# Performance work log

Measured on AMD Instinct MI355X. Metric: run time of the kernel, lower is better.

## Reference

```python
import jax, jax.numpy as jnp
import numpy as np

B, S, D_IN, D_OUT = 8, 2048, 1024, 1024

def setup_inputs() -> dict:
    key = jax.random.key(0)
    k1, k2, k3, k4 = jax.random.split(key, 4)
    sc = 0.02
    return {
        "x": jax.random.normal(k1, (B, S, D_IN), dtype=jnp.float32),
        "Wq": jax.random.normal(k2, (D_IN, D_OUT), dtype=jnp.float32) * sc,
        "Wk": jax.random.normal(k3, (D_IN, D_OUT), dtype=jnp.float32) * sc,
        "Wv": jax.random.normal(k4, (D_IN, D_OUT), dtype=jnp.float32) * sc,
    }

def reference(x, Wq, Wk, Wv):
    b, n, _ = x.shape
    d_out = Wq.shape[1]
    q = jnp.einsum('bsd,de->bse', x, Wq)   # [b, n, d_out]
    k = jnp.einsum('bsd,de->bse', x, Wk)
    v = jnp.einsum('bsd,de->bse', x, Wv)
    scores = jnp.einsum('bie,bje->bij', q, k)  # [b, n, n]
    # causal mask: positions j > i set to -inf (triu, diagonal=1)
    causal = jnp.triu(jnp.ones((n, n), dtype=bool), k=1)
    scores = jnp.where(causal[None, :, :], -jnp.inf, scores)
    # NOTE: source applies softmax over dim=1 (query axis), scaled by sqrt(d_out)
    weights = jax.nn.softmax(scores / jnp.sqrt(jnp.float32(d_out)), axis=1)
    # dropout is identity in eval mode (p=0)
    return jnp.einsum('bij,bje->bie', weights, v)
```

## Files before the change

kernel.cpp:

```cpp
#include <hip/hip_runtime.h>
#include <hip/hip_bf16.h>


using bf16 = __hip_bfloat16;
typedef __attribute__((ext_vector_type(8))) short short8;
typedef __attribute__((ext_vector_type(4))) float f32x4;

__device__ __forceinline__ float bfbits2f(unsigned short u) {
  return __uint_as_float((unsigned)u << 16);
}

__global__ void cvt_kernel(const float* __restrict__ in, bf16* __restrict__ out) {
  size_t i = ((size_t)blockIdx.x * 256 + threadIdx.x) * 4;
  float4 v = *(const float4*)(in + i);
  alignas(8) bf16 h[4] = {__float2bfloat16(v.x), __float2bfloat16(v.y),
                          __float2bfloat16(v.z), __float2bfloat16(v.w)};
  *(unsigned long long*)(out + i) = *(const unsigned long long*)h;
}

__global__ void pre_kernel(const float* __restrict__ x,
                           const float* __restrict__ W0, const float* __restrict__ W1,
                           const float* __restrict__ W2, bf16* __restrict__ Wt,
                           float* __restrict__ lbuf, bf16* __restrict__ Xb) {
  int tid = threadIdx.x;
  int zz = blockIdx.z;
  if (zz == 3) {
    int bid = blockIdx.y * 16 + blockIdx.x;
    if (bid < 64) lbuf[bid * 256 + tid] = 0.f;
    return;
  }
  if (zz >= 4) {
    size_t cb = (size_t)(zz - 4) * 256 + blockIdx.y * 16 + blockIdx.x;
    size_t i = (cb * 256 + tid) * 4;
    float4 v = *(const float4*)(x + i);
    alignas(8) bf16 h[4] = {__float2bfloat16(v.x), __float2bfloat16(v.y),
                            __float2bfloat16(v.z), __float2bfloat16(v.w)};
    *(unsigned long long*)(Xb + i) = *(const unsigned long long*)h;
    return;
  }
  const float* W = zz == 0 ? W0 : zz == 1 ? W1 : W2;
  bf16* O = Wt + (size_t)zz * 1048576ull;
  __shared__ float t[64][65];
  int n0 = blockIdx.x * 64, k0 = blockIdx.y * 64;
#pragma unroll
  for (int i = 0; i < 4; ++i) {
    int idx = i * 1024 + tid * 4;
    int r = idx >> 6, c = idx & 63;
    float4 v = *(const float4*)(W + (size_t)(k0 + r) * 1024 + n0 + c);
    t[r][c] = v.x; t[r][c + 1] = v.y; t[r][c + 2] = v.z; t[r][c + 3] = v.w;
  }
  __syncthreads();
#pragma unroll
  for (int i = 0; i < 4; ++i) {
    int idx = i * 1024 + tid * 4;
    int r = idx >> 6, c = idx & 63;
    alignas(8) bf16 h[4] = {__float2bfloat16(t[c][r]), __float2bfloat16(t[c + 1][r]),
                            __float2bfloat16(t[c + 2][r]), __float2bfloat16(t[c + 3][r])};
    *(unsigned long long*)(O + (size_t)(n0 + r) * 1024 + k0 + c) = *(const unsigned long long*)h;
  }
}

__global__ void vhat_kernel(const bf16* __restrict__ QKV, const float* __restrict__ l,
                            bf16* __restrict__ Vt) {
  int lb = blockIdx.z;
  const unsigned short* V =
      (const unsigned short*)QKV + ((size_t)lb * 3 + 2) * 2097152ull;
  bf16* O = Vt + (size_t)lb * 2097152ull;
  const float* lc = l + lb * 2048;
  __shared__ float t[64][65];
  __shared__ float rl[64];
  int j0 = blockIdx.x * 64, e0 = blockIdx.y * 64;
  int tid = threadIdx.x;
  if (tid < 64) rl[tid] = 1.0f / lc[j0 + tid];
#pragma unroll
  for (int i = 0; i < 4; ++i) {
    int idx = i * 1024 + tid * 4;
    int r = idx >> 6, c = idx & 63;
    ushort4 u = *(const ushort4*)(V + (size_t)(j0 + r) * 1024 + e0 + c);
    t[r][c] = bfbits2f(u.x); t[r][c + 1] = bfbits2f(u.y);
    t[r][c + 2] = bfbits2f(u.z); t[r][c + 3] = bfbits2f(u.w);
  }
  __syncthreads();
#pragma unroll
  for (int i = 0; i < 4; ++i) {
    int idx = i * 1024 + tid * 4;
    int r = idx >> 6, c = idx & 63;
    alignas(8) bf16 h[4] = {
        __float2bfloat16(t[c][r] * rl[c]), __float2bfloat16(t[c + 1][r] * rl[c + 1]),
        __float2bfloat16(t[c + 2][r] * rl[c + 2]), __float2bfloat16(t[c + 3][r] * rl[c + 3])};
    *(unsigned long long*)(O + (size_t)(e0 + r) * 2048 + j0 + c) = *(const unsigned long long*)h;
  }
}

template <int EPI, bool VARK, bool TRI>
__device__ __forceinline__ void gemm_bt_body(
    const bf16* __restrict__ A, const bf16* __restrict__ B, void* __restrict__ Cv,
    int lda, int ldb, int ldc, int Kin, int zdivA, int zmodB,
    unsigned long long sA, unsigned long long sB, unsigned long long sC,
    float* __restrict__ lptr) {
  unsigned bz, bx, by;
  if constexpr (TRI) {
    const unsigned gx = gridDim.x;
    const unsigned total = gx * gridDim.z;
    unsigned id = blockIdx.x + gx * blockIdx.z;
    unsigned lid = (id & 7) * (total >> 3) + (id >> 3);
    bz = lid / gx;
    unsigned t = lid - bz * gx;
    int r = (int)((__builtin_sqrtf(8.f * (float)t + 1.f) - 1.f) * 0.5f);
    while ((r + 1) * (r + 2) / 2 <= (int)t) ++r;
    while (r * (r + 1) / 2 > (int)t) --r;
    by = (unsigned)r;
    bx = t - (unsigned)(r * (r + 1) / 2);
  } else {
    const unsigned gx = gridDim.x, gy = gridDim.y;
    const unsigned per_z = gx * gy;
    const unsigned total = per_z * gridDim.z;
    unsigned id = blockIdx.x + gx * (blockIdx.y + gy * blockIdx.z);
    unsigned lid = (id & 7) * (total >> 3) + (id >> 3);
    bz = lid / per_z;
    unsigned rem = lid - bz * per_z;
    constexpr unsigned H = 8;
    const unsigned band = rem / (gx * H);
    const unsigned w = rem - band * (gx * H);
    bx = w / H;
    const unsigned by_raw = band * H + (w - bx * H);
    by = VARK ? (gy - 1 - by_raw) : by_raw;
  }

  const int z = (int)bz;
  A += (unsigned long long)(z / zdivA) * sA;
  B += (unsigned long long)(z % zmodB) * sB;
  const int K = VARK ? (int)(by + 1) * 128 : Kin;

  alignas(16) __shared__ bf16 As[128 * 64];
  alignas(16) __shared__ bf16 Bs[128 * 64];

  const int tid = threadIdx.x, wave = tid >> 6, lane = tid & 63;
  const int m0 = by * 128, n0 = bx * 128;
  const int srow = tid >> 3;
  const int scol_g = ((tid & 7) ^ (srow & 7)) * 8;
  const int scol_l = (tid & 7) * 8;
  const int wm = (wave >> 1) * 64, wn = (wave & 1) * 64;
  const int fm = lane & 15, sw = lane & 7, kg = lane >> 4;

  f32x4 acc[4][4];
#pragma unroll
  for (int mi = 0; mi < 4; ++mi)
#pragma unroll
    for (int ni = 0; ni < 4; ++ni) acc[mi][ni] = (f32x4){0.f, 0.f, 0.f, 0.f};

  const bf16* Arow = A + (size_t)m0 * lda;
  const bf16* Brow = B + (size_t)n0 * ldb;

  for (int k0 = 0; k0 < K; k0 += 64) {
    __syncthreads();
#pragma unroll
    for (int c = 0; c < 4; ++c) {
      int row = c * 32 + srow;
      __builtin_amdgcn_global_load_lds(
          (const __attribute__((address_space(1))) void*)(Arow + (size_t)row * lda + k0 + scol_g),
          (__attribute__((address_space(3))) void*)(As + row * 64 + scol_l), 16, 0, 0);
    }
#pragma unroll
    for (int c = 0; c < 4; ++c) {
      int row = c * 32 + srow;
      __builtin_amdgcn_global_load_lds(
          (const __attribute__((address_space(1))) void*)(Brow + (size_t)row * ldb + k0 + scol_g),
          (__attribute__((address_space(3))) void*)(Bs + row * 64 + scol_l), 16, 0, 0);
    }
    __syncthreads();
#pragma unroll
    for (int ks = 0; ks < 2; ++ks) {
      const int pc = ((ks * 4 + kg) ^ sw) * 8;
      short8 af[4], bf_[4];
#pragma unroll
      for (int i = 0; i < 4; ++i) {
        af[i] = *(const short8*)(As + (wm + i * 16 + fm) * 64 + pc);
        bf_[i] = *(const short8*)(Bs + (wn + i * 16 + fm) * 64 + pc);
      }
#pragma unroll
      for (int mi = 0; mi < 4; ++mi)
#pragma unroll
        for (int ni = 0; ni < 4; ++ni)
          acc[mi][ni] = __builtin_amdgcn_mfma_f32_16x16x32_bf16(af[mi], bf_[ni], acc[mi][ni], 0, 0, 0);
    }
  }

  const int cr = kg * 4, cc = fm;
  if constexpr (EPI == 2) {
    float* C = (float*)Cv + (unsigned long long)z * sC;
#pragma unroll
    for (int mi = 0; mi < 4; ++mi)
#pragma unroll
      for (int ni = 0; ni < 4; ++ni)
#pragma unroll
        for (int r = 0; r < 4; ++r)
          C[(size_t)(m0 + wm + mi * 16 + cr + r) * ldc + (n0 + wn + ni * 16 + cc)] = acc[mi][ni][r];
  } else if constexpr (EPI == 0) {
    bf16* C = (bf16*)Cv + (unsigned long long)z * sC;
#pragma unroll
    for (int mi = 0; mi < 4; ++mi)
#pragma unroll
      for (int ni = 0; ni < 4; ++ni)
#pragma unroll
        for (int r = 0; r < 4; ++r)
          C[(size_t)(m0 + wm + mi * 16 + cr + r) * ldc + (n0 + wn + ni * 16 + cc)] =
              __float2bfloat16(acc[mi][ni][r]);
  } else {
    bf16* C = (bf16*)Cv + (unsigned long long)z * sC;
    float colpart[4] = {0.f, 0.f, 0.f, 0.f};
#pragma unroll
    for (int mi = 0; mi < 4; ++mi)
#pragma unroll
      for (int ni = 0; ni < 4; ++ni)
#pragma unroll
        for (int r = 0; r < 4; ++r) {
          int gm = m0 + wm + mi * 16 + cr + r;
          int gn = n0 + wn + ni * 16 + cc;
          float s = acc[mi][ni][r] * 0.03125f;
          float p = (gn <= gm) ? __expf(s) : 0.f;
          colpart[ni] += p;
          C[(size_t)gm * ldc + gn] = __float2bfloat16(p);
        }
    float* lcol = lptr + (size_t)z * 2048 + n0 + wn;
#pragma unroll
    for (int ni = 0; ni < 4; ++ni) {
      float s = colpart[ni];
      s += __shfl_xor(s, 16);
      s += __shfl_xor(s, 32);
      if (lane < 16) atomicAdd(&lcol[ni * 16 + lane], s);
    }
  }
}

__global__ __launch_bounds__(256, 4) void gemm_qkv(
    const bf16* __restrict__ A, const bf16* __restrict__ B, void* __restrict__ Cv,
    int lda, int ldb, int ldc, int Kin, int zdivA, int zmodB,
    unsigned long long sA, unsigned long long sB, unsigned long long sC) {
  gemm_bt_body<0, false, false>(A, B, Cv, lda, ldb, ldc, Kin, zdivA, zmodB, sA, sB, sC, nullptr);
}
__global__ __launch_bounds__(256, 4) void gemm_scores(
    const bf16* __restrict__ A, const bf16* __restrict__ B, void* __restrict__ Cv,
    int lda, int ldb, int ldc, int Kin, int zdivA, int zmodB,
    unsigned long long sA, unsigned long long sB, unsigned long long sC,
    float* __restrict__ lptr) {
  gemm_bt_body<1, false, true>(A, B, Cv, lda, ldb, ldc, Kin, zdivA, zmodB, sA, sB, sC, lptr);
}
__global__ __launch_bounds__(256, 4) void gemm_pv(
    const bf16* __restrict__ A, const bf16* __restrict__ B, void* __restrict__ Cv,
    int lda, int ldb, int ldc, int Kin, int zdivA, int zmodB,
    unsigned long long sA, unsigned long long sB, unsigned long long sC) {
  gemm_bt_body<2, true, false>(A, B, Cv, lda, ldb, ldc, Kin, zdivA, zmodB, sA, sB, sC, nullptr);
}

extern "C" void kernel_launch(void* const* d_in, const int* in_sizes, int n_in,
                              void* d_out, int out_size, void* d_ws, size_t ws_size,
                              hipStream_t stream) {
  const float* x = (const float*)d_in[0];
  const float* Wq = (const float*)d_in[1];
  const float* Wk = (const float*)d_in[2];
  const float* Wv = (const float*)d_in[3];
  float* out = (float*)d_out;

  constexpr unsigned long long X_EL = 2048ull * 1024;
  constexpr unsigned long long QKV_EL = 3ull * X_EL;
  constexpr unsigned long long P_EL = 2048ull * 2048;
  constexpr unsigned long long VT_EL = 1024ull * 2048;
  constexpr unsigned long long WT_B = 3ull * 1024 * 1024 * 2;
  constexpr unsigned long long LB_B = 8ull * 2048 * 4;
  constexpr unsigned long long PER_B = 2 * (X_EL + QKV_EL + P_EL + VT_EL);

  size_t NB = 1;
  for (size_t nb : {(size_t)8, (size_t)4, (size_t)2})
    if (WT_B + LB_B + nb * PER_B <= ws_size) { NB = nb; break; }

  char* p = (char*)d_ws;
  bf16* Wt = (bf16*)p;   p += WT_B;
  float* lbuf = (float*)p; p += LB_B;
  bf16* Xb = (bf16*)p;   p += 2 * NB * X_EL;
  bf16* QKV = (bf16*)p;  p += 2 * NB * QKV_EL;
  bf16* P = (bf16*)p;    p += 2 * NB * P_EL;
  bf16* Vt = (bf16*)p;

  pre_kernel<<<dim3(16, 16, (unsigned)(4 + NB * 8)), 256, 0, stream>>>(
      x, Wq, Wk, Wv, Wt, lbuf, Xb);

  for (size_t b0 = 0; b0 < 8; b0 += NB) {
    if (b0)
      cvt_kernel<<<dim3((unsigned)(NB * 2048)), 256, 0, stream>>>(x + b0 * X_EL, Xb);
    const size_t nbA = NB / 2, nbB = NB - nbA;
    if (nbA)
      gemm_qkv<<<dim3(8, 16, (unsigned)(nbA * 3)), 256, 0, stream>>>(
          Xb, Wt, QKV, 1024, 1024, 1024, 1024, 3, 3, X_EL, 1048576ull, X_EL);
    gemm_qkv<<<dim3(8, 16, (unsigned)(nbB * 3)), 256, 0, stream>>>(
        Xb + nbA * X_EL, Wt, QKV + nbA * QKV_EL, 1024, 1024, 1024, 1024, 3, 3,
        X_EL, 1048576ull, X_EL);
    gemm_scores<<<dim3(136, 1, (unsigned)NB), 256, 0, stream>>>(
        QKV, QKV + X_EL, P, 1024, 1024, 2048, 1024, 1, 1 << 30, QKV_EL, QKV_EL, P_EL,
        lbuf + b0 * 2048);
    vhat_kernel<<<dim3(32, 16, (unsigned)NB), 256, 0, stream>>>(QKV, lbuf + b0 * 2048, Vt);
    gemm_pv<<<dim3(8, 16, (unsigned)NB), 256, 0, stream>>>(
        P, Vt, out + b0 * X_EL, 2048, 2048, 1024, 0, 1, 1 << 30, P_EL, VT_EL, X_EL);
  }
}
```

Measured before the change: 341.7 us.

## Pair triangular row tiles in PV GEMM for balanced work per block

Rewrites the PV GEMM as a dedicated kernel with 128x64 tiles, where each block handles two row tiles (15-p and p) of the causal P matrix. Every block therefore does a constant total K length instead of the earlier varying-K 128x128 tiles, which removes tail imbalance. It also merges the two split QKV GEMM launches into one. The cost is smaller N tiles, which means less B reuse per block and more A reloads, plus a smaller accumulator tile.

```diff
diff --git a/kernel.cpp b/kernel.cpp
--- a/kernel.cpp
+++ b/kernel.cpp
@@ -92,7 +92,7 @@
   }
 }
 
-template <int EPI, bool VARK, bool TRI>
+template <int EPI, bool TRI>
 __device__ __forceinline__ void gemm_bt_body(
     const bf16* __restrict__ A, const bf16* __restrict__ B, void* __restrict__ Cv,
     int lda, int ldb, int ldc, int Kin, int zdivA, int zmodB,
@@ -123,14 +123,13 @@
     const unsigned band = rem / (gx * H);
     const unsigned w = rem - band * (gx * H);
     bx = w / H;
-    const unsigned by_raw = band * H + (w - bx * H);
-    by = VARK ? (gy - 1 - by_raw) : by_raw;
+    by = band * H + (w - bx * H);
   }
 
   const int z = (int)bz;
   A += (unsigned long long)(z / zdivA) * sA;
   B += (unsigned long long)(z % zmodB) * sB;
-  const int K = VARK ? (int)(by + 1) * 128 : Kin;
+  const int K = Kin;
 
   alignas(16) __shared__ bf16 As[128 * 64];
   alignas(16) __shared__ bf16 Bs[128 * 64];
@@ -187,16 +186,7 @@
   }
 
   const int cr = kg * 4, cc = fm;
-  if constexpr (EPI == 2) {
-    float* C = (float*)Cv + (unsigned long long)z * sC;
-#pragma unroll
-    for (int mi = 0; mi < 4; ++mi)
-#pragma unroll
-      for (int ni = 0; ni < 4; ++ni)
-#pragma unroll
-        for (int r = 0; r < 4; ++r)
-          C[(size_t)(m0 + wm + mi * 16 + cr + r) * ldc + (n0 + wn + ni * 16 + cc)] = acc[mi][ni][r];
-  } else if constexpr (EPI == 0) {
+  if constexpr (EPI == 0) {
     bf16* C = (bf16*)Cv + (unsigned long long)z * sC;
 #pragma unroll
     for (int mi = 0; mi < 4; ++mi)
@@ -237,20 +227,102 @@
     const bf16* __restrict__ A, const bf16* __restrict__ B, void* __restrict__ Cv,
     int lda, int ldb, int ldc, int Kin, int zdivA, int zmodB,
     unsigned long long sA, unsigned long long sB, unsigned long long sC) {
-  gemm_bt_body<0, false, false>(A, B, Cv, lda, ldb, ldc, Kin, zdivA, zmodB, sA, sB, sC, nullptr);
+  gemm_bt_body<0, false>(A, B, Cv, lda, ldb, ldc, Kin, zdivA, zmodB, sA, sB, sC, nullptr);
 }
 __global__ __launch_bounds__(256, 4) void gemm_scores(
     const bf16* __restrict__ A, const bf16* __restrict__ B, void* __restrict__ Cv,
     int lda, int ldb, int ldc, int Kin, int zdivA, int zmodB,
     unsigned long long sA, unsigned long long sB, unsigned long long sC,
     float* __restrict__ lptr) {
-  gemm_bt_body<1, false, true>(A, B, Cv, lda, ldb, ldc, Kin, zdivA, zmodB, sA, sB, sC, lptr);
-}
+  gemm_bt_body<1, true>(A, B, Cv, lda, ldb, ldc, Kin, zdivA, zmodB, sA, sB, sC, lptr);
+}
+
 __global__ __launch_bounds__(256, 4) void gemm_pv(
-    const bf16* __restrict__ A, const bf16* __restrict__ B, void* __restrict__ Cv,
-    int lda, int ldb, int ldc, int Kin, int zdivA, int zmodB,
+    const bf16* __restrict__ Pm, const bf16* __restrict__ Vt, float* __restrict__ out,
     unsigned long long sA, unsigned long long sB, unsigned long long sC) {
-  gemm_bt_body<2, true, false>(A, B, Cv, lda, ldb, ldc, Kin, zdivA, zmodB, sA, sB, sC, nullptr);
+  const unsigned gx = gridDim.x, gy = gridDim.y;
+  const unsigned per_z = gx * gy;
+  const unsigned total = per_z * gridDim.z;
+  unsigned id = blockIdx.x + gx * (blockIdx.y + gy * blockIdx.z);
+  unsigned lid = (id & 7) * (total >> 3) + (id >> 3);
+  const unsigned bz = lid / per_z;
+  unsigned rem = lid - bz * per_z;
+  const unsigned bx = rem >> 3;
+  const unsigned pp = rem & 7;
+  const int z = (int)bz;
+
+  const bf16* A = Pm + (unsigned long long)z * sA;
+  const bf16* B = Vt + (unsigned long long)z * sB;
+  float* C = out + (unsigned long long)z * sC;
+
+  alignas(16) __shared__ bf16 As[128 * 64];
+  alignas(16) __shared__ bf16 Bs[64 * 64];
+
+  const int tid = threadIdx.x, wave = tid >> 6, lane = tid & 63;
+  const int srow = tid >> 3;
+  const int scol_g = ((tid & 7) ^ (srow & 7)) * 8;
+  const int scol_l = (tid & 7) * 8;
+  const int wm = (wave >> 1) * 64, wn = (wave & 1) * 32;
+  const int fm = lane & 15, sw = lane & 7, kg = lane >> 4;
+  const int n0 = (int)bx * 64;
+  const bf16* Brow = B + (size_t)n0 * 2048;
+
+  auto phase = [&](int by, int K) {
+    const int m0 = by * 128;
+    const bf16* Arow = A + (size_t)m0 * 2048;
+    f32x4 acc[4][2];
+#pragma unroll
+    for (int mi = 0; mi < 4; ++mi)
+#pragma unroll
+      for (int nj = 0; nj < 2; ++nj) acc[mi][nj] = (f32x4){0.f, 0.f, 0.f, 0.f};
+
+    for (int k0 = 0; k0 < K; k0 += 64) {
+      __syncthreads();
+#pragma unroll
+      for (int c = 0; c < 4; ++c) {
+        int row = c * 32 + srow;
+        __builtin_amdgcn_global_load_lds(
+            (const __attribute__((address_space(1))) void*)(Arow + (size_t)row * 2048 + k0 + scol_g),
+            (__attribute__((address_space(3))) void*)(As + row * 64 + scol_l), 16, 0, 0);
+      }
+#pragma unroll
+      for (int c = 0; c < 2; ++c) {
+        int row = c * 32 + srow;
+        __builtin_amdgcn_global_load_lds(
+            (const __attribute__((address_space(1))) void*)(Brow + (size_t)row * 2048 + k0 + scol_g),
+            (__attribute__((address_space(3))) void*)(Bs + row * 64 + scol_l), 16, 0, 0);
+      }
+      __syncthreads();
+#pragma unroll
+      for (int ks = 0; ks < 2; ++ks) {
+        const int pc = ((ks * 4 + kg) ^ sw) * 8;
+        short8 af[4], bf_[2];
+#pragma unroll
+        for (int i = 0; i < 4; ++i)
+          af[i] = *(const short8*)(As + (wm + i * 16 + fm) * 64 + pc);
+#pragma unroll
+        for (int j = 0; j < 2; ++j)
+          bf_[j] = *(const short8*)(Bs + (wn + j * 16 + fm) * 64 + pc);
+#pragma unroll
+        for (int mi = 0; mi < 4; ++mi)
+#pragma unroll
+          for (int nj = 0; nj < 2; ++nj)
+            acc[mi][nj] = __builtin_amdgcn_mfma_f32_16x16x32_bf16(af[mi], bf_[nj], acc[mi][nj], 0, 0, 0);
+      }
+    }
+    const int cr = kg * 4, cc = fm;
+#pragma unroll
+    for (int mi = 0; mi < 4; ++mi)
+#pragma unroll
+      for (int nj = 0; nj < 2; ++nj)
+#pragma unroll
+        for (int r = 0; r < 4; ++r)
+          C[(size_t)(m0 + wm + mi * 16 + cr + r) * 1024 + (n0 + wn + nj * 16 + cc)] =
+              acc[mi][nj][r];
+  };
+
+  phase(15 - (int)pp, (16 - (int)pp) * 128);
+  phase((int)pp, ((int)pp + 1) * 128);
 }
 
 extern "C" void kernel_launch(void* const* d_in, const int* in_sizes, int n_in,
@@ -288,18 +360,13 @@
   for (size_t b0 = 0; b0 < 8; b0 += NB) {
     if (b0)
       cvt_kernel<<<dim3((unsigned)(NB * 2048)), 256, 0, stream>>>(x + b0 * X_EL, Xb);
-    const size_t nbA = NB / 2, nbB = NB - nbA;
-    if (nbA)
-      gemm_qkv<<<dim3(8, 16, (unsigned)(nbA * 3)), 256, 0, stream>>>(
-          Xb, Wt, QKV, 1024, 1024, 1024, 1024, 3, 3, X_EL, 1048576ull, X_EL);
-    gemm_qkv<<<dim3(8, 16, (unsigned)(nbB * 3)), 256, 0, stream>>>(
-        Xb + nbA * X_EL, Wt, QKV + nbA * QKV_EL, 1024, 1024, 1024, 1024, 3, 3,
-        X_EL, 1048576ull, X_EL);
+    gemm_qkv<<<dim3(8, 16, (unsigned)(NB * 3)), 256, 0, stream>>>(
+        Xb, Wt, QKV, 1024, 1024, 1024, 1024, 3, 3, X_EL, 1048576ull, X_EL);
     gemm_scores<<<dim3(136, 1, (unsigned)NB), 256, 0, stream>>>(
         QKV, QKV + X_EL, P, 1024, 1024, 2048, 1024, 1, 1 << 30, QKV_EL, QKV_EL, P_EL,
         lbuf + b0 * 2048);
     vhat_kernel<<<dim3(32, 16, (unsigned)NB), 256, 0, stream>>>(QKV, lbuf + b0 * 2048, Vt);
-    gemm_pv<<<dim3(8, 16, (unsigned)NB), 256, 0, stream>>>(
-        P, Vt, out + b0 * X_EL, 2048, 2048, 1024, 0, 1, 1 << 30, P_EL, VT_EL, X_EL);
-  }
-}
+    gemm_pv<<<dim3(16, 8, (unsigned)NB), 256, 0, stream>>>(
+        P, Vt, out + b0 * X_EL, P_EL, VT_EL, X_EL);
+  }
+}
```

Measured after the change: 324.3 us. -5.1%, faster.
